# Optimization experiments

Measured on AMD Instinct MI355X. Metric: run time of the kernel, lower is better.

Reference implementation:

```python
import jax, jax.numpy as jnp
import numpy as np

N_WIRES = 25                    # odd -> RX on wire 0, then SingleExcitation on (1,2),(3,4),...,(23,24)
DIM = 2 ** N_WIRES              # 33_554_432 amplitudes
N_THETA = (N_WIRES + 1) // 2    # 13


def _apply_rx(state, th, wire):
    """Apply RX(th) = [[cos, -i sin], [-i sin, cos]] (half-angle) to `wire`.
    PennyLane convention: wire 0 is the most-significant bit of the amplitude index."""
    c = jnp.cos(th * 0.5)
    ms = -1j * jnp.sin(th * 0.5)
    st = state.reshape(2 ** wire, 2, -1)          # [pre, 2, post]
    s0, s1 = st[:, 0], st[:, 1]
    new = jnp.stack([c * s0 + ms * s1, ms * s0 + c * s1], axis=1)
    return new.reshape(-1)


def _apply_single_excitation(state, phi, wire):
    """SingleExcitation(phi) on wires [wire, wire+1]: rotates the |01>,|10> subspace
    by angle phi/2; |00>,|11> untouched."""
    c = jnp.cos(phi * 0.5)
    s = jnp.sin(phi * 0.5)
    st = state.reshape(2 ** wire, 2, 2, -1)       # [pre, q_i, q_{i+1}, post]
    a00, a01, a10, a11 = st[:, 0, 0], st[:, 0, 1], st[:, 1, 0], st[:, 1, 1]
    n01 = c * a01 - s * a10
    n10 = s * a01 + c * a10
    new = jnp.stack([jnp.stack([a00, n01], axis=1),
                     jnp.stack([n10, a11], axis=1)], axis=1)
    return new.reshape(-1)


def setup_inputs() -> dict:
    key = jax.random.key(0)
    kf, kt = jax.random.split(key)
    feature = jax.random.normal(kf, (DIM,), dtype=jnp.float32)
    # he_normal init on shape (13, 1): std = sqrt(2 / fan_in) with fan_in = 13
    theta = jax.random.normal(kt, (N_THETA, 1), dtype=jnp.float32) * np.sqrt(2.0 / N_THETA)
    return {"feature": feature, "theta": theta}


def reference(feature, theta) -> jnp.ndarray:
    # AmplitudeEmbedding with pad_with=0.0: pad (no-op here, len == 2^n) then L2-normalize
    state = (feature / jnp.linalg.norm(feature)).astype(jnp.complex64)
    # odd wire count: RX(theta[0][0]) on wire 0, start pair gates at wire 1
    state = _apply_rx(state, theta[0, 0], 0)
    for i in range(1, N_WIRES, 2):                # i = 1,3,...,23 -> theta[0..11]
        state = _apply_single_excitation(state, theta[i // 2, 0], i)
    return jnp.real(state)
```

## Files before the change

### kernel.cpp

```cpp
#include <hip/hip_runtime.h>
#include <math.h>


typedef float f32x4 __attribute__((ext_vector_type(4)));

static __device__ __forceinline__ float4 nt_load4(const float* p) {
    f32x4 v = __builtin_nontemporal_load((const f32x4*)p);
    return *(float4*)&v;
}
static __device__ __forceinline__ void nt_store4(float* p, float4 v) {
    __builtin_nontemporal_store(*(f32x4*)&v, (f32x4*)p);
}

static __device__ __forceinline__ void bar_lgkm() {
    asm volatile("s_waitcnt lgkmcnt(0)\n\ts_barrier" ::: "memory");
}

static __device__ __forceinline__ void rot4(float4& a, float4& b, float c, float s) {
    float4 na, nb;
    na.x = c*a.x - s*b.x;  nb.x = s*a.x + c*b.x;
    na.y = c*a.y - s*b.y;  nb.y = s*a.y + c*b.y;
    na.z = c*a.z - s*b.z;  nb.z = s*a.z + c*b.z;
    na.w = c*a.w - s*b.w;  nb.w = s*a.w + c*b.w;
    a = na; b = nb;
}

static __device__ __forceinline__ float4 shflx4(float4 v, int m) {
    float4 r;
    r.x = __shfl_xor(v.x, m, 64);
    r.y = __shfl_xor(v.y, m, 64);
    r.z = __shfl_xor(v.z, m, 64);
    r.w = __shfl_xor(v.w, m, 64);
    return r;
}

template <int NR>
static __device__ __forceinline__ void rotshfl(float4* f, int sh, float c, float s, int lane) {
    const int pv = (lane >> sh) & 3;
    const bool act = (pv == 1) || (pv == 2);
    const float cl = act ? c : 1.0f;
    const float sl = act ? ((pv == 1) ? -s : s) : 0.0f;
    const int m = 3 << sh;
#pragma unroll
    for (int k = 0; k < NR; ++k) {
        float4 p = shflx4(f[k], m);
        float4 n;
        n.x = fmaf(sl, p.x, cl * f[k].x);
        n.y = fmaf(sl, p.y, cl * f[k].y);
        n.z = fmaf(sl, p.z, cl * f[k].z);
        n.w = fmaf(sl, p.w, cl * f[k].w);
        f[k] = n;
    }
}

static __device__ __forceinline__ float sumsq16(const float4* f) {
    float q[16];
#pragma unroll
    for (int k = 0; k < 16; ++k)
        q[k] = fmaf(f[k].x, f[k].x,
               fmaf(f[k].y, f[k].y,
               fmaf(f[k].z, f[k].z, f[k].w * f[k].w)));
#pragma unroll
    for (int st = 1; st < 16; st <<= 1)
#pragma unroll
        for (int i = 0; i < 16; i += (st << 1))
            q[i] += q[i + st];
    return q[0];
}

__global__ __launch_bounds__(256, 2) void qnn_p1(const float* __restrict__ in,
                                                 const float* __restrict__ theta,
                                                 float* __restrict__ out,
                                                 double* __restrict__ partials) {
    __shared__ __align__(16) float4 lds[4096];
    __shared__ double red[4];
    const int t = threadIdx.x, lane = t & 63, w2 = t >> 6;
    const long gA = (long)blockIdx.x << 13;
    const long gB = gA + 4096;

    float c0,s0,c1,s1,c2,s2,c3,s3,c4,s4,c5,s5,c6,s6;
    { float th;
      th=0.5f*theta[11]; c0=cosf(th); s0=sinf(th);
      th=0.5f*theta[10]; c1=cosf(th); s1=sinf(th);
      th=0.5f*theta[9];  c2=cosf(th); s2=sinf(th);
      th=0.5f*theta[8];  c3=cosf(th); s3=sinf(th);
      th=0.5f*theta[7];  c4=cosf(th); s4=sinf(th);
      th=0.5f*theta[6];  c5=cosf(th); s5=sinf(th);
      th=0.5f*theta[5];  c6=cosf(th); s6=sinf(th); }

    float4 f[16], g[16];
#pragma unroll
    for (int k = 0; k < 16; ++k)
        f[k] = nt_load4(in + ((gA + ((w2 << 10) | (k << 6) | lane)) << 2));
#pragma unroll
    for (int k = 0; k < 16; ++k)
        g[k] = nt_load4(in + ((gB + ((w2 << 10) | (k << 6) | lane)) << 2));

    const float sA = sumsq16(f);

#pragma unroll
    for (int k = 0; k < 16; ++k) {
        float ny = c0*f[k].y - s0*f[k].z;
        float nz = s0*f[k].y + c0*f[k].z;
        f[k].y = ny; f[k].z = nz;
    }
    rotshfl<16>(f, 0, c1, s1, lane);
    rotshfl<16>(f, 2, c2, s2, lane);
    rotshfl<16>(f, 4, c3, s3, lane);
#pragma unroll
    for (int hi = 0; hi < 16; hi += 4) rot4(f[hi+1], f[hi+2], c4, s4);
#pragma unroll
    for (int lo = 0; lo < 4; ++lo)     rot4(f[4+lo], f[8+lo], c5, s5);

#pragma unroll
    for (int k = 0; k < 16; ++k) lds[(w2 << 10) | (k << 6) | lane] = f[k];
    bar_lgkm();
#pragma unroll
    for (int m = 0; m < 16; ++m) f[m] = lds[(m << 8) | (w2 << 6) | lane];
#pragma unroll
    for (int lo = 0; lo < 4; ++lo) rot4(f[4+lo], f[8+lo], c6, s6);
#pragma unroll
    for (int m = 0; m < 16; ++m)
        *(float4*)(out + ((gA + ((m << 8) | (w2 << 6) | lane)) << 2)) = f[m];

    const float sB = sumsq16(g);
#pragma unroll
    for (int k = 0; k < 16; ++k) {
        float ny = c0*g[k].y - s0*g[k].z;
        float nz = s0*g[k].y + c0*g[k].z;
        g[k].y = ny; g[k].z = nz;
    }
    rotshfl<16>(g, 0, c1, s1, lane);
    rotshfl<16>(g, 2, c2, s2, lane);
    rotshfl<16>(g, 4, c3, s3, lane);
#pragma unroll
    for (int hi = 0; hi < 16; hi += 4) rot4(g[hi+1], g[hi+2], c4, s4);
#pragma unroll
    for (int lo = 0; lo < 4; ++lo)     rot4(g[4+lo], g[8+lo], c5, s5);

    bar_lgkm();
#pragma unroll
    for (int k = 0; k < 16; ++k) lds[(w2 << 10) | (k << 6) | lane] = g[k];
    bar_lgkm();
#pragma unroll
    for (int m = 0; m < 16; ++m) g[m] = lds[(m << 8) | (w2 << 6) | lane];
#pragma unroll
    for (int lo = 0; lo < 4; ++lo) rot4(g[4+lo], g[8+lo], c6, s6);
#pragma unroll
    for (int m = 0; m < 16; ++m)
        *(float4*)(out + ((gB + ((m << 8) | (w2 << 6) | lane)) << 2)) = g[m];

    double acc = (double)sA + (double)sB;
#pragma unroll
    for (int off = 32; off > 0; off >>= 1) acc += __shfl_down(acc, off, 64);
    if (lane == 0) red[w2] = acc;
    bar_lgkm();
    if (t == 0)
        partials[blockIdx.x] = red[0] + red[1] + red[2] + red[3];
}

__global__ void qnn_norm(const double* __restrict__ partials,
                         const float* __restrict__ theta,
                         double* __restrict__ scale) {
    __shared__ double w[4];
    const int t = threadIdx.x;
    double acc = 0.0;
    for (int i = t; i < 1024; i += 256) acc += partials[i];
#pragma unroll
    for (int off = 32; off > 0; off >>= 1) acc += __shfl_down(acc, off, 64);
    if ((t & 63) == 0) w[t >> 6] = acc;
    __syncthreads();
    if (t == 0) {
        double tot = w[0] + w[1] + w[2] + w[3];
        *scale = (double)cosf(0.5f * theta[0]) / sqrt(tot);
    }
}

__global__ __launch_bounds__(512, 2) void qnn_high(float* __restrict__ buf,
                                                   const float* __restrict__ theta,
                                                   const double* __restrict__ scale) {
    __shared__ __align__(16) float4 lds[8192];
    const int t = threadIdx.x, lane = t & 63, w3 = t >> 6;
    const int mid = blockIdx.x;
    const long gqA = (long)mid << 3;
    const long gqB = (1L << 22) | ((long)mid << 3);

    float c7,s7,c8,s8,c9,s9,c10,s10,c11,s11;
    { float th;
      th=0.5f*theta[4]; c7 =cosf(th); s7 =sinf(th);
      th=0.5f*theta[3]; c8 =cosf(th); s8 =sinf(th);
      th=0.5f*theta[2]; c9 =cosf(th); s9 =sinf(th);
      th=0.5f*theta[1]; c10=cosf(th); s10=sinf(th);
      th=0.5f*theta[0]; c11=cosf(th); s11=sinf(th); }
    const float sc = (float)(*scale);

    const int rbase = (w3 << 10) | ((lane >> 5) << 9) | (lane & 31);

    float4 f[16], g[16];
#pragma unroll
    for (int k = 0; k < 16; ++k) {
        const int s_ = (k << 9) | t;
        f[k] = *(const float4*)(buf + ((gqA | ((long)(s_ >> 3) << 12) | (s_ & 7)) << 2));
    }
#pragma unroll
    for (int k = 0; k < 16; ++k) {
        const int s_ = (k << 9) | t;
        g[k] = *(const float4*)(buf + ((gqB | ((long)(s_ >> 3) << 12) | (s_ & 7)) << 2));
    }

    rotshfl<16>(f, 3, c7, s7, lane);
#pragma unroll
    for (int hi = 0; hi < 16; hi += 4) rot4(f[hi+1], f[hi+2], c10, s10);
#pragma unroll
    for (int lo = 0; lo < 4; ++lo)     rot4(f[4+lo], f[8+lo], c11, s11);
#pragma unroll
    for (int k = 0; k < 16; ++k) lds[(k << 9) | t] = f[k];
    bar_lgkm();
#pragma unroll
    for (int m = 0; m < 16; ++m) f[m] = lds[rbase | (m << 5)];
#pragma unroll
    for (int hi = 0; hi < 16; hi += 4) rot4(f[hi+1], f[hi+2], c8, s8);
#pragma unroll
    for (int lo = 0; lo < 4; ++lo)     rot4(f[4+lo], f[8+lo], c9, s9);
#pragma unroll
    for (int m = 0; m < 16; ++m) {
        const int s_ = rbase | (m << 5);
        float4 v = f[m];
        v.x *= sc; v.y *= sc; v.z *= sc; v.w *= sc;
        nt_store4(buf + ((gqA | ((long)(s_ >> 3) << 12) | (s_ & 7)) << 2), v);
    }

    rotshfl<16>(g, 3, c7, s7, lane);
#pragma unroll
    for (int hi = 0; hi < 16; hi += 4) rot4(g[hi+1], g[hi+2], c10, s10);
#pragma unroll
    for (int lo = 0; lo < 4; ++lo)     rot4(g[4+lo], g[8+lo], c11, s11);
    bar_lgkm();
#pragma unroll
    for (int k = 0; k < 16; ++k) lds[(k << 9) | t] = g[k];
    bar_lgkm();
#pragma unroll
    for (int m = 0; m < 16; ++m) g[m] = lds[rbase | (m << 5)];
#pragma unroll
    for (int hi = 0; hi < 16; hi += 4) rot4(g[hi+1], g[hi+2], c8, s8);
#pragma unroll
    for (int lo = 0; lo < 4; ++lo)     rot4(g[4+lo], g[8+lo], c9, s9);
#pragma unroll
    for (int m = 0; m < 16; ++m) {
        const int s_ = rbase | (m << 5);
        float4 v = g[m];
        v.x *= sc; v.y *= sc; v.z *= sc; v.w *= sc;
        nt_store4(buf + ((gqB | ((long)(s_ >> 3) << 12) | (s_ & 7)) << 2), v);
    }
}

extern "C" void kernel_launch(void* const* d_in, const int* in_sizes, int n_in,
                              void* d_out, int out_size, void* d_ws, size_t ws_size,
                              hipStream_t stream) {
    const float* in = (const float*)d_in[0];
    const float* theta = (const float*)d_in[1];
    float* out = (float*)d_out;
    double* part = (double*)d_ws;
    double* scale = part + 1024;

    qnn_p1<<<1024, 256, 0, stream>>>(in, theta, out, part);
    qnn_norm<<<1, 256, 0, stream>>>(part, theta, scale);
    qnn_high<<<512, 512, 0, stream>>>(out, theta, scale);
}
```

Measured before the change: 97.54 us.

## Remap high-wire kernel tiles so f/g halves pair across a wire boundary

```diff
diff --git a/kernel.cpp b/kernel.cpp
--- a/kernel.cpp
+++ b/kernel.cpp
@@ -180,10 +180,11 @@
                                                    const float* __restrict__ theta,
                                                    const double* __restrict__ scale) {
     __shared__ __align__(16) float4 lds[8192];
-    const int t = threadIdx.x, lane = t & 63, w3 = t >> 6;
-    const int mid = blockIdx.x;
-    const long gqA = (long)mid << 3;
-    const long gqB = (1L << 22) | ((long)mid << 3);
+    const int t = threadIdx.x, lane = t & 63;
+    const int bid = blockIdx.x;
+    const int b24 = bid >> 8, mid = bid & 255;
+    const long baseA = ((long)b24 << 22) | ((long)mid << 4);
+    const long baseB = baseA | (1L << 21);
 
     float c7,s7,c8,s8,c9,s9,c10,s10,c11,s11;
     { float th;
@@ -194,63 +195,70 @@
       th=0.5f*theta[0]; c11=cosf(th); s11=sinf(th); }
     const float sc = (float)(*scale);
 
-    const int rbase = (w3 << 10) | ((lane >> 5) << 9) | (lane & 31);
-
     float4 f[16], g[16];
 #pragma unroll
     for (int k = 0; k < 16; ++k) {
         const int s_ = (k << 9) | t;
-        f[k] = *(const float4*)(buf + ((gqA | ((long)(s_ >> 3) << 12) | (s_ & 7)) << 2));
+        f[k] = *(const float4*)(buf + ((baseA | ((long)(s_ >> 4) << 12) | (s_ & 15)) << 2));
     }
 #pragma unroll
     for (int k = 0; k < 16; ++k) {
         const int s_ = (k << 9) | t;
-        g[k] = *(const float4*)(buf + ((gqB | ((long)(s_ >> 3) << 12) | (s_ & 7)) << 2));
-    }
-
-    rotshfl<16>(f, 3, c7, s7, lane);
-#pragma unroll
-    for (int hi = 0; hi < 16; hi += 4) rot4(f[hi+1], f[hi+2], c10, s10);
-#pragma unroll
-    for (int lo = 0; lo < 4; ++lo)     rot4(f[4+lo], f[8+lo], c11, s11);
+        g[k] = *(const float4*)(buf + ((baseB | ((long)(s_ >> 4) << 12) | (s_ & 15)) << 2));
+    }
+
+    rotshfl<16>(f, 4, c7, s7, lane);
+    rotshfl<16>(g, 4, c7, s7, lane);
+#pragma unroll
+    for (int h8 = 0; h8 < 16; h8 += 8) {
+        rot4(f[h8+2], f[h8+4], c10, s10);
+        rot4(f[h8+3], f[h8+5], c10, s10);
+        rot4(g[h8+2], g[h8+4], c10, s10);
+        rot4(g[h8+3], g[h8+5], c10, s10);
+    }
+#pragma unroll
+    for (int i = 0; i < 8; ++i)
+        rot4(f[8+i], g[i], c11, s11);
+
 #pragma unroll
     for (int k = 0; k < 16; ++k) lds[(k << 9) | t] = f[k];
     bar_lgkm();
-#pragma unroll
-    for (int m = 0; m < 16; ++m) f[m] = lds[rbase | (m << 5)];
-#pragma unroll
-    for (int hi = 0; hi < 16; hi += 4) rot4(f[hi+1], f[hi+2], c8, s8);
-#pragma unroll
-    for (int lo = 0; lo < 4; ++lo)     rot4(f[4+lo], f[8+lo], c9, s9);
-#pragma unroll
-    for (int m = 0; m < 16; ++m) {
-        const int s_ = rbase | (m << 5);
-        float4 v = f[m];
-        v.x *= sc; v.y *= sc; v.z *= sc; v.w *= sc;
-        nt_store4(buf + ((gqA | ((long)(s_ >> 3) << 12) | (s_ & 7)) << 2), v);
-    }
-
-    rotshfl<16>(g, 3, c7, s7, lane);
-#pragma unroll
-    for (int hi = 0; hi < 16; hi += 4) rot4(g[hi+1], g[hi+2], c10, s10);
-#pragma unroll
-    for (int lo = 0; lo < 4; ++lo)     rot4(g[4+lo], g[8+lo], c11, s11);
-    bar_lgkm();
+    {
+        const int rb = ((t >> 6) << 10) | (t & 63);
+#pragma unroll
+        for (int m = 0; m < 16; ++m) f[m] = lds[rb | (m << 6)];
+#pragma unroll
+        for (int q = 0; q < 16; q += 4) rot4(f[q+1], f[q+2], c8, s8);
+#pragma unroll
+        for (int lo = 0; lo < 4; ++lo)  rot4(f[4+lo], f[8+lo], c9, s9);
+#pragma unroll
+        for (int m = 0; m < 16; ++m) {
+            const int s_ = rb | (m << 6);
+            float4 v = f[m];
+            v.x *= sc; v.y *= sc; v.z *= sc; v.w *= sc;
+            nt_store4(buf + ((baseA | ((long)(s_ >> 4) << 12) | (s_ & 15)) << 2), v);
+        }
+    }
+    bar_lgkm();
+
 #pragma unroll
     for (int k = 0; k < 16; ++k) lds[(k << 9) | t] = g[k];
     bar_lgkm();
-#pragma unroll
-    for (int m = 0; m < 16; ++m) g[m] = lds[rbase | (m << 5)];
-#pragma unroll
-    for (int hi = 0; hi < 16; hi += 4) rot4(g[hi+1], g[hi+2], c8, s8);
-#pragma unroll
-    for (int lo = 0; lo < 4; ++lo)     rot4(g[4+lo], g[8+lo], c9, s9);
-#pragma unroll
-    for (int m = 0; m < 16; ++m) {
-        const int s_ = rbase | (m << 5);
-        float4 v = g[m];
-        v.x *= sc; v.y *= sc; v.z *= sc; v.w *= sc;
-        nt_store4(buf + ((gqB | ((long)(s_ >> 3) << 12) | (s_ & 7)) << 2), v);
+    {
+        const int rb = ((t >> 6) << 10) | (t & 63);
+#pragma unroll
+        for (int m = 0; m < 16; ++m) g[m] = lds[rb | (m << 6)];
+#pragma unroll
+        for (int q = 0; q < 16; q += 4) rot4(g[q+1], g[q+2], c8, s8);
+#pragma unroll
+        for (int lo = 0; lo < 4; ++lo)  rot4(g[4+lo], g[8+lo], c9, s9);
+#pragma unroll
+        for (int m = 0; m < 16; ++m) {
+            const int s_ = rb | (m << 6);
+            float4 v = g[m];
+            v.x *= sc; v.y *= sc; v.z *= sc; v.w *= sc;
+            nt_store4(buf + ((baseB | ((long)(s_ >> 4) << 12) | (s_ & 15)) << 2), v);
+        }
     }
 }
 
```

Result: faster. 93.53 us, median of 2 (-4.1%).
